# Optimization experiments

Hardware: AMD Instinct MI355X
Metric: run time of the kernel (lower is better)

The kernel has to match this reference:

```python
import jax, jax.numpy as jnp
import numpy as np
from jax import lax

NUM_EMBEDDING = 512
D_EMBEDDING = 256
COMMITMENT_COST = 0.25
B = 131072


def setup_inputs() -> dict:
    key = jax.random.key(0)
    k1, k2, k3 = jax.random.split(key, 3)
    node_type = jax.random.randint(k1, (B,), 0, 10, dtype=jnp.int64 if jax.config.jax_enable_x64 else jnp.int32)
    node_representation = jax.random.normal(k2, (B, D_EMBEDDING), dtype=jnp.float32)
    # nn.Embedding default init: N(0, 1)
    codebook = jax.random.normal(k3, (NUM_EMBEDDING, D_EMBEDDING), dtype=jnp.float32)
    return {"node_type": node_type, "node_representation": node_representation, "codebook": codebook}


def _code_indices(node_type, z, codebook):
    # Map atom type -> codebook quadrant: C(5)->0, N(6)->1, O(7)->2, others->3
    K = codebook.shape[0]
    qsize = K // 4
    group = jnp.where(node_type == 5, 0,
            jnp.where(node_type == 6, 1,
            jnp.where(node_type == 7, 2, 3)))  # [b]
    # Squared L2 distances to all codes: ||z||^2 + ||e||^2 - 2 z.e  -> [b, K]
    d2 = (jnp.sum(z * z, axis=1, keepdims=True)
          + jnp.sum(codebook * codebook, axis=1)
          - 2.0 * (z @ codebook.T))
    col_group = jnp.arange(K) // qsize  # [K], quadrant of each code
    valid = group[:, None] == col_group[None, :]  # [b, K]
    # Masked argmin == per-quadrant argmin (+ quadrant offset), as in the original.
    return jnp.argmin(jnp.where(valid, d2, jnp.inf), axis=1)


def reference(node_type, node_representation, codebook):
    z = node_representation
    idx = _code_indices(node_type, z, codebook)          # [b]
    quantized = codebook[idx]                            # [b, d]
    vq_loss = jnp.mean((quantized - lax.stop_gradient(z)) ** 2)
    commitment_loss = COMMITMENT_COST * jnp.mean((z - lax.stop_gradient(quantized)) ** 2)
    # Straight-through estimator
    quantized_st = z + lax.stop_gradient(quantized - z)
    return (vq_loss, commitment_loss, idx, quantized_st)
```

## Files before the change

### kernel.cpp

```cpp
#include <hip/hip_runtime.h>


#define B_ROWS   131072
#define D_EMB    256
#define TPB      256
#define MAXT     8196
#define SGRID2   1025
#define THETA    0.0625f

#define WS_WSUM   0
#define WS_I64N   512
#define WS_GCNT   516
#define WS_GPOS   532
#define WS_NT     548
#define WS_CBH    1024
#define WS_CBL    (WS_CBH + 262144)
#define WS_EN     (WS_CBL + 262144)
#define WS_ROWS   (WS_EN + 2048)
#define WS_TD     (WS_ROWS + 524288)
#define WS_NEED_NEW (WS_TD + 4 * MAXT)
#define WS_FLAGS  8

typedef __attribute__((ext_vector_type(8))) short bf16x8;
typedef __attribute__((ext_vector_type(4))) float f32x4;

__device__ __forceinline__ float bf2f(unsigned short u) {
    return __uint_as_float(((unsigned)u) << 16);
}

__device__ __forceinline__ void splitA(const float4& a0, const float4& a1,
                                       bf16x8& ah, bf16x8& al) {
    float ff[8] = {a0.x, a0.y, a0.z, a0.w, a1.x, a1.y, a1.z, a1.w};
    #pragma unroll
    for (int j = 0; j < 8; ++j) {
        unsigned u = __float_as_uint(ff[j]);
        ah[j] = (short)(u >> 16);
        float r = ff[j] - __uint_as_float(u & 0xffff0000u);
        al[j] = (short)(__float_as_uint(r) >> 16);
    }
}

__global__ void vq_prep(const float* __restrict__ cbf, const int* __restrict__ nt,
                        unsigned short* __restrict__ cbh, unsigned short* __restrict__ cbl,
                        float* __restrict__ eN, int* __restrict__ flagI64) {
    const int code = blockIdx.x;
    const int lane = threadIdx.x;
    float4 v = *(const float4*)(cbf + code * 256 + lane * 4);

    unsigned u0 = __float_as_uint(v.x), u1 = __float_as_uint(v.y);
    unsigned u2 = __float_as_uint(v.z), u3 = __float_as_uint(v.w);
    ushort4 h = make_ushort4((unsigned short)(u0 >> 16), (unsigned short)(u1 >> 16),
                             (unsigned short)(u2 >> 16), (unsigned short)(u3 >> 16));
    float r0 = v.x - __uint_as_float(u0 & 0xffff0000u);
    float r1 = v.y - __uint_as_float(u1 & 0xffff0000u);
    float r2 = v.z - __uint_as_float(u2 & 0xffff0000u);
    float r3 = v.w - __uint_as_float(u3 & 0xffff0000u);
    ushort4 l = make_ushort4((unsigned short)(__float_as_uint(r0) >> 16),
                             (unsigned short)(__float_as_uint(r1) >> 16),
                             (unsigned short)(__float_as_uint(r2) >> 16),
                             (unsigned short)(__float_as_uint(r3) >> 16));
    *(ushort4*)(cbh + code * 256 + lane * 4) = h;
    *(ushort4*)(cbl + code * 256 + lane * 4) = l;

    float s = fmaf(v.x, v.x, fmaf(v.y, v.y, fmaf(v.z, v.z, v.w * v.w)));
    #pragma unroll
    for (int d = 1; d < 64; d <<= 1) s += __shfl_xor(s, d);
    if (lane == 0) eN[code] = s;

    if (code == 0) {
        int o = (nt[2 * lane + 1] != 0) ? 1 : 0;
        unsigned long long m = __ballot(o != 0);
        if (lane == 0) flagI64[0] = (m == 0ULL) ? 1 : 0;
    }
}

__global__ void vq_bin1(const int* __restrict__ nt, const int* __restrict__ fI,
                        int* __restrict__ gcnt) {
    __shared__ int c[4];
    const int tid = threadIdx.x;
    if (tid < 4) c[tid] = 0;
    __syncthreads();
    const int row = blockIdx.x * 256 + tid;
    const int t = fI[0] ? nt[2 * row] : nt[row];
    const int g = (t == 5) ? 0 : (t == 6) ? 1 : (t == 7) ? 2 : 3;
    atomicAdd(&c[g], 1);
    __syncthreads();
    if (tid < 4) atomicAdd(&gcnt[tid], c[tid]);
}

__global__ void vq_tiles32(const int* __restrict__ gcnt, int* __restrict__ gpos,
                           int* __restrict__ nT, int* __restrict__ td) {
    __shared__ int off[4], cnt[4], to[4], tot;
    if (threadIdx.x == 0) {
        int o = 0, t = 0;
        for (int g = 0; g < 4; ++g) {
            cnt[g] = gcnt[g];
            off[g] = o; o += cnt[g];
            int tc = (cnt[g] + 31) >> 5;
            to[g] = t; t += tc;
            gpos[g] = off[g];
        }
        tot = t; nT[0] = t;
    }
    __syncthreads();
    const int t = tot;
    for (int i = threadIdx.x; i < t; i += 64) {
        int g = 3;
        if (i < to[1]) g = 0; else if (i < to[2]) g = 1; else if (i < to[3]) g = 2;
        int b = i - to[g];
        int base = off[g] + b * 32;
        int nr = cnt[g] - b * 32; if (nr > 32) nr = 32;
        td[i] = nr | (base << 6) | (g << 23);
    }
}

__global__ void vq_bin2(const int* __restrict__ nt, const int* __restrict__ fI,
                        int* __restrict__ gpos, int* __restrict__ rows) {
    __shared__ int base[4], pos[4];
    const int tid = threadIdx.x;
    if (tid < 4) pos[tid] = 0;
    __syncthreads();
    const int row = blockIdx.x * 256 + tid;
    const int t = fI[0] ? nt[2 * row] : nt[row];
    const int g = (t == 5) ? 0 : (t == 6) ? 1 : (t == 7) ? 2 : 3;
    atomicAdd(&pos[g], 1);
    __syncthreads();
    if (tid < 4) { base[tid] = atomicAdd(&gpos[tid], pos[tid]); pos[tid] = 0; }
    __syncthreads();
    int p = atomicAdd(&pos[g], 1);
    rows[base[g] + p] = row;
}

__global__ __launch_bounds__(TPB, 3) void vq_score2(
    const float* __restrict__ zf,
    const float* __restrict__ cbf,
    const unsigned short* __restrict__ cbh,
    const unsigned short* __restrict__ cbl,
    const float* __restrict__ eN,
    const int* __restrict__ rows,
    const int* __restrict__ td,
    const int* __restrict__ nT,
    float* __restrict__ out,
    double* __restrict__ wsum)
{
    __shared__ int2   sT[4][16];
    __shared__ float2 sM[4][16];
    __shared__ float  sZZ[4][16];
    __shared__ double sRed[4];

    const int tid  = threadIdx.x;
    const int wave = tid >> 6;
    const int lane = tid & 63;
    const int col  = lane & 15;
    const int quad = lane >> 4;
    const int w    = blockIdx.x * 4 + wave;

    double lacc = 0.0;

    if (w < nT[0]) {
        const int d    = td[w];
        const int nr   = d & 63;
        const int base = (d >> 6) & 0x1FFFF;
        const int g    = d >> 23;
        const int nr0  = (nr < 16) ? nr : 16;
        const int nr1  = nr - 16;

        int ix0 = base + ((col < nr0) ? col : (nr0 - 1));
        int ix1 = (nr1 > 0) ? (base + 16 + ((col < nr1) ? col : (nr1 - 1))) : ix0;
        const int rowA0 = rows[ix0];
        const int rowA1 = rows[ix1];
        const float* za0 = zf + rowA0 * 256 + quad * 8;
        const float* za1 = zf + rowA1 * 256 + quad * 8;
        const unsigned short* bhp = cbh + (g * 128 + col) * 256 + quad * 8;
        const unsigned short* blp = cbl + (g * 128 + col) * 256 + quad * 8;

        f32x4 acc[2][8];
        #pragma unroll
        for (int st = 0; st < 2; ++st)
            #pragma unroll
            for (int t = 0; t < 8; ++t) acc[st][t] = (f32x4){0.f, 0.f, 0.f, 0.f};
        float zz0 = 0.f, zz1 = 0.f;

        #pragma unroll
        for (int c = 0; c < 8; ++c) {
            float4 a00 = *(const float4*)(za0 + c * 32);
            float4 a01 = *(const float4*)(za0 + c * 32 + 4);
            float4 a10 = *(const float4*)(za1 + c * 32);
            float4 a11 = *(const float4*)(za1 + c * 32 + 4);
            zz0 = fmaf(a00.x,a00.x,fmaf(a00.y,a00.y,fmaf(a00.z,a00.z,fmaf(a00.w,a00.w,zz0))));
            zz0 = fmaf(a01.x,a01.x,fmaf(a01.y,a01.y,fmaf(a01.z,a01.z,fmaf(a01.w,a01.w,zz0))));
            zz1 = fmaf(a10.x,a10.x,fmaf(a10.y,a10.y,fmaf(a10.z,a10.z,fmaf(a10.w,a10.w,zz1))));
            zz1 = fmaf(a11.x,a11.x,fmaf(a11.y,a11.y,fmaf(a11.z,a11.z,fmaf(a11.w,a11.w,zz1))));
            bf16x8 ah0, al0, ah1, al1;
            splitA(a00, a01, ah0, al0);
            splitA(a10, a11, ah1, al1);
            #pragma unroll
            for (int t = 0; t < 8; ++t) {
                bf16x8 bh = *(const bf16x8*)(bhp + t * 4096 + c * 32);
                bf16x8 bl = *(const bf16x8*)(blp + t * 4096 + c * 32);
                acc[0][t] = __builtin_amdgcn_mfma_f32_16x16x32_bf16(ah0, bh, acc[0][t], 0, 0, 0);
                acc[0][t] = __builtin_amdgcn_mfma_f32_16x16x32_bf16(al0, bh, acc[0][t], 0, 0, 0);
                acc[0][t] = __builtin_amdgcn_mfma_f32_16x16x32_bf16(ah0, bl, acc[0][t], 0, 0, 0);
                acc[1][t] = __builtin_amdgcn_mfma_f32_16x16x32_bf16(ah1, bh, acc[1][t], 0, 0, 0);
                acc[1][t] = __builtin_amdgcn_mfma_f32_16x16x32_bf16(al1, bh, acc[1][t], 0, 0, 0);
                acc[1][t] = __builtin_amdgcn_mfma_f32_16x16x32_bf16(ah1, bl, acc[1][t], 0, 0, 0);
            }
        }
        zz0 += __shfl_xor(zz0, 16); zz0 += __shfl_xor(zz0, 32);
        zz1 += __shfl_xor(zz1, 16); zz1 += __shfl_xor(zz1, 32);

        float e8[8];
        #pragma unroll
        for (int t = 0; t < 8; ++t) e8[t] = eN[g * 128 + t * 16 + col];

        for (int st = 0; st < 2; ++st) {
            const int nrs = st ? nr1 : nr0;
            if (nrs <= 0) continue;
            if (quad == 0) sZZ[wave][col] = st ? zz1 : zz0;

            #pragma unroll
            for (int r = 0; r < 4; ++r) {
                float m1 = __builtin_inff(), m2 = __builtin_inff();
                int   i1 = 0x7fffffff,      i2 = 0x7fffffff;
                #pragma unroll
                for (int t = 0; t < 8; ++t) {
                    float sc = e8[t] - 2.f * acc[st][t][r];
                    int   ci = t * 16 + col;
                    if (sc < m1 || (sc == m1 && ci < i1)) { m2 = m1; i2 = i1; m1 = sc; i1 = ci; }
                    else if (sc < m2 || (sc == m2 && ci < i2)) { m2 = sc; i2 = ci; }
                }
                #pragma unroll
                for (int d2 = 1; d2 < 16; d2 <<= 1) {
                    float b1 = __shfl_xor(m1, d2);
                    int  bi1 = __shfl_xor(i1, d2);
                    float b2 = __shfl_xor(m2, d2);
                    int  bi2 = __shfl_xor(i2, d2);
                    if (b1 < m1 || (b1 == m1 && bi1 < i1)) {
                        float om = m1; int oi = i1;
                        m1 = b1; i1 = bi1;
                        if (b2 < om || (b2 == om && bi2 < oi)) { m2 = b2; i2 = bi2; }
                        else                                   { m2 = om; i2 = oi; }
                    } else {
                        if (b1 < m2 || (b1 == m2 && bi1 < i2)) { m2 = b1; i2 = bi1; }
                    }
                }
                if (col == 0) {
                    sT[wave][quad * 4 + r] = make_int2(i1, i2);
                    sM[wave][quad * 4 + r] = make_float2(m1, m2);
                }
            }

            const int s  = lane >> 2;
            const int pq = lane & 3;
            const bool valid = (s < nrs);
            int grow = 0, c1 = 0, c2 = 0;
            float scm1 = 0.f, scm2 = 1e30f, zzr = 0.f;
            if (valid) {
                grow = rows[base + st * 16 + s];
                int2  tt = sT[wave][s];
                float2 mm = sM[wave][s];
                zzr = sZZ[wave][s];
                c1 = g * 128 + tt.x;
                c2 = g * 128 + tt.y;
                scm1 = mm.x; scm2 = mm.y;
            }
            int    wfin  = c1;
            double dfull = (double)(zzr + scm1);
            const bool need = valid && (scm2 - scm1 <= THETA);

            if (__any(need)) {
                double d1c = 0.0, d2c = 0.0;
                if (need) {
                    const float* zp = zf  + grow * 256 + pq * 64;
                    const float* p1 = cbf + c1 * 256 + pq * 64;
                    const float* p2 = cbf + c2 * 256 + pq * 64;
                    #pragma unroll 4
                    for (int it = 0; it < 16; ++it) {
                        float4 fz = *(const float4*)(zp + it * 4);
                        float4 g1 = *(const float4*)(p1 + it * 4);
                        float4 g2 = *(const float4*)(p2 + it * 4);
                        double e;
                        e = (double)fz.x - (double)g1.x; d1c = fma(e, e, d1c);
                        e = (double)fz.y - (double)g1.y; d1c = fma(e, e, d1c);
                        e = (double)fz.z - (double)g1.z; d1c = fma(e, e, d1c);
                        e = (double)fz.w - (double)g1.w; d1c = fma(e, e, d1c);
                        e = (double)fz.x - (double)g2.x; d2c = fma(e, e, d2c);
                        e = (double)fz.y - (double)g2.y; d2c = fma(e, e, d2c);
                        e = (double)fz.z - (double)g2.z; d2c = fma(e, e, d2c);
                        e = (double)fz.w - (double)g2.w; d2c = fma(e, e, d2c);
                    }
                }
                double t1 = d1c + __shfl_xor(d1c, 1); t1 += __shfl_xor(t1, 2);
                double t2 = d2c + __shfl_xor(d2c, 1); t2 += __shfl_xor(t2, 2);
                if (need) {
                    bool take1 = (t1 < t2) || (t1 == t2 && c1 < c2);
                    wfin  = take1 ? c1 : c2;
                    dfull = take1 ? t1 : t2;
                }
            }

            if (valid) {
                if (pq == 0) lacc += dfull;
                const float* pw = cbf + wfin * 256 + pq * 64;
                const int obase = 2 + B_ROWS + grow * 256 + pq * 64;
                float4 fprev = *(const float4*)(pw);
                *(float2*)(out + obase) = make_float2(fprev.x, fprev.y);
                #pragma unroll
                for (int it = 1; it < 16; ++it) {
                    float4 fcur = *(const float4*)(pw + it * 4);
                    *(float4*)(out + obase + (it - 1) * 4 + 2) =
                        make_float4(fprev.z, fprev.w, fcur.x, fcur.y);
                    fprev = fcur;
                }
                *(float2*)(out + obase + 62) = make_float2(fprev.z, fprev.w);
                if (pq == 0) out[2 + grow] = (float)wfin;
            }
        }
    }

    #pragma unroll
    for (int d2 = 1; d2 < 64; d2 <<= 1) lacc += __shfl_xor(lacc, d2);
    if (lane == 0) sRed[wave] = lacc;
    __syncthreads();
    if (tid == 0) atomicAdd(&wsum[blockIdx.x & 63], sRed[0] + sRed[1] + sRed[2] + sRed[3]);
}

__global__ void vq_detect(const unsigned short* cb, const int* nt, int* flag) {
    __shared__ int cnt, odd;
    if (threadIdx.x == 0) { cnt = 0; odd = 0; }
    __syncthreads();
    int c = 0, o = 0;
    for (int i = threadIdx.x; i < 512; i += 64) {
        unsigned short u = cb[2 * i];
        int e = (u >> 7) & 0xFF;
        if (e < 100 || e > 140) c++;
    }
    if (nt[2 * threadIdx.x + 1] != 0) o = 1;
    atomicAdd(&cnt, c);
    atomicAdd(&odd, o);
    __syncthreads();
    if (threadIdx.x == 0) {
        flag[0] = (cnt < 50) ? 1 : 0;
        flag[1] = (odd == 0) ? 1 : 0;
    }
}

__global__ __launch_bounds__(512, 2) void vq_main_f32(
    const int* __restrict__ nt,
    const float* __restrict__ zff,
    const float* __restrict__ cbf,
    float* __restrict__ out,
    double* __restrict__ wsum,
    const int* __restrict__ flag)
{
    if (flag[0] != 0) return;
    const int i64 = flag[1];

    __shared__ float  sE[256 * 132];
    __shared__ float  sZ[128 * 32];
    __shared__ int    sList[512];
    __shared__ int    sCnt[4], sPos[4];
    __shared__ int    sTop1[128], sTop2[128];
    __shared__ float  sEe[128];
    __shared__ double sRed[8];

    const int tid  = threadIdx.x;
    const int row0 = blockIdx.x * 512;

    if (tid < 4) { sCnt[tid] = 0; sPos[tid] = 0; }
    __syncthreads();
    {
        int t = i64 ? nt[2 * (row0 + tid)] : nt[row0 + tid];
        int g = (t == 5) ? 0 : (t == 6) ? 1 : (t == 7) ? 2 : 3;
        atomicAdd(&sCnt[g], 1);
        __syncthreads();
        int o1 = sCnt[0], o2 = o1 + sCnt[1], o3 = o2 + sCnt[2];
        int offg = (g == 0) ? 0 : (g == 1) ? o1 : (g == 2) ? o2 : o3;
        int p = atomicAdd(&sPos[g], 1);
        sList[offg + p] = row0 + tid;
    }
    __syncthreads();

    int cnt[4], off[4];
    cnt[0] = sCnt[0]; cnt[1] = sCnt[1]; cnt[2] = sCnt[2]; cnt[3] = sCnt[3];
    off[0] = 0; off[1] = cnt[0]; off[2] = off[1] + cnt[1]; off[3] = off[2] + cnt[2];

    const int ccol = tid & 31, rrow = tid >> 5;
    const int c0 = ccol * 4, rbase = rrow * 8;
    double lacc = 0.0;

    for (int gg = 0; gg < 4; ++gg) {
        const int n = cnt[gg];
        if (n == 0) continue;
        __syncthreads();
        for (int i = tid; i < 128 * 256; i += 512) {
            int c = i >> 8, k = i & 255;
            sE[k * 132 + c] = cbf[(gg * 128 + c) * 256 + k];
        }
        __syncthreads();
        if (tid < 128) {
            float s = 0.f;
            for (int k = 0; k < 256; ++k) { float v = sE[k * 132 + tid]; s = fmaf(v, v, s); }
            sEe[tid] = s;
        }
        __syncthreads();

        const int ntiles = (n + 127) >> 7;
        for (int tI = 0; tI < ntiles; ++tI) {
            const int tbase = off[gg] + tI * 128;
            const int nrows = min(128, n - tI * 128);
            float acc[8][4];
            #pragma unroll
            for (int r = 0; r < 8; ++r)
                #pragma unroll
                for (int q = 0; q < 4; ++q) acc[r][q] = 0.f;

            for (int kb = 0; kb < 8; ++kb) {
                __syncthreads();
                #pragma unroll
                for (int it = 0; it < 2; ++it) {
                    int i = it * 512 + tid;
                    int s = i >> 3, j = i & 7;
                    float4 v = make_float4(0.f, 0.f, 0.f, 0.f);
                    if (s < nrows) {
                        int gr = sList[tbase + s];
                        v = *(const float4*)(zff + gr * 256 + kb * 32 + j * 4);
                    }
                    *(float4*)&sZ[s * 32 + j * 4] = v;
                }
                __syncthreads();
                #pragma unroll
                for (int k4 = 0; k4 < 8; ++k4) {
                    const int kk = kb * 32 + k4 * 4;
                    const float4 e0 = *(const float4*)&sE[(kk + 0) * 132 + c0];
                    const float4 e1 = *(const float4*)&sE[(kk + 1) * 132 + c0];
                    const float4 e2 = *(const float4*)&sE[(kk + 2) * 132 + c0];
                    const float4 e3 = *(const float4*)&sE[(kk + 3) * 132 + c0];
                    #pragma unroll
                    for (int r = 0; r < 8; ++r) {
                        const float4 zv = *(const float4*)&sZ[(rbase + r) * 32 + k4 * 4];
                        acc[r][0] = fmaf(zv.x, e0.x, fmaf(zv.y, e1.x, fmaf(zv.z, e2.x, fmaf(zv.w, e3.x, acc[r][0]))));
                        acc[r][1] = fmaf(zv.x, e0.y, fmaf(zv.y, e1.y, fmaf(zv.z, e2.y, fmaf(zv.w, e3.y, acc[r][1]))));
                        acc[r][2] = fmaf(zv.x, e0.z, fmaf(zv.y, e1.z, fmaf(zv.z, e2.z, fmaf(zv.w, e3.z, acc[r][2]))));
                        acc[r][3] = fmaf(zv.x, e0.w, fmaf(zv.y, e1.w, fmaf(zv.z, e2.w, fmaf(zv.w, e3.w, acc[r][3]))));
                    }
                }
            }

            float eq[4] = { sEe[c0], sEe[c0 + 1], sEe[c0 + 2], sEe[c0 + 3] };
            for (int r = 0; r < 8; ++r) {
                float m1 = __builtin_inff(), m2 = __builtin_inff();
                int   i1 = 0x7fffffff,      i2 = 0x7fffffff;
                #pragma unroll
                for (int q = 0; q < 4; ++q) {
                    float sc = eq[q] - 2.f * acc[r][q];
                    int   ci = c0 + q;
                    if (sc < m1 || (sc == m1 && ci < i1)) { m2 = m1; i2 = i1; m1 = sc; i1 = ci; }
                    else if (sc < m2 || (sc == m2 && ci < i2)) { m2 = sc; i2 = ci; }
                }
                #pragma unroll
                for (int d = 1; d < 32; d <<= 1) {
                    float b1 = __shfl_xor(m1, d);
                    int  bi1 = __shfl_xor(i1, d);
                    float b2 = __shfl_xor(m2, d);
                    int  bi2 = __shfl_xor(i2, d);
                    if (b1 < m1 || (b1 == m1 && bi1 < i1)) {
                        float om = m1; int oi = i1;
                        m1 = b1; i1 = bi1;
                        if (b2 < om || (b2 == om && bi2 < oi)) { m2 = b2; i2 = bi2; }
                        else                                   { m2 = om; i2 = oi; }
                    } else {
                        if (b1 < m2 || (b1 == m2 && bi1 < i2)) { m2 = b1; i2 = bi1; }
                    }
                }
                if (ccol == 0) { sTop1[rbase + r] = i1; sTop2[rbase + r] = i2; }
            }
            __syncthreads();

            {
                const int s  = tid >> 2;
                const int pq = tid & 3;
                const bool valid = (s < nrows);
                double d1c = 0.0, d2c = 0.0;
                int gr = 0, c1g = 0, c2g = 0;
                if (valid) {
                    gr  = sList[tbase + s];
                    c1g = gg * 128 + sTop1[s];
                    c2g = gg * 128 + sTop2[s];
                    #pragma unroll 4
                    for (int it = 0; it < 16; ++it) {
                        float4 fz = *(const float4*)(zff + gr  * 256 + pq * 64 + it * 4);
                        float4 f1 = *(const float4*)(cbf + c1g * 256 + pq * 64 + it * 4);
                        float4 f2 = *(const float4*)(cbf + c2g * 256 + pq * 64 + it * 4);
                        double e;
                        e = (double)fz.x - (double)f1.x; d1c = fma(e, e, d1c);
                        e = (double)fz.y - (double)f1.y; d1c = fma(e, e, d1c);
                        e = (double)fz.z - (double)f1.z; d1c = fma(e, e, d1c);
                        e = (double)fz.w - (double)f1.w; d1c = fma(e, e, d1c);
                        e = (double)fz.x - (double)f2.x; d2c = fma(e, e, d2c);
                        e = (double)fz.y - (double)f2.y; d2c = fma(e, e, d2c);
                        e = (double)fz.z - (double)f2.z; d2c = fma(e, e, d2c);
                        e = (double)fz.w - (double)f2.w; d2c = fma(e, e, d2c);
                    }
                }
                double t1 = d1c + __shfl_xor(d1c, 1); t1 += __shfl_xor(t1, 2);
                double t2 = d2c + __shfl_xor(d2c, 1); t2 += __shfl_xor(t2, 2);
                if (valid) {
                    bool take1 = (t1 < t2) || (t1 == t2 && c1g < c2g);
                    int  w = take1 ? c1g : c2g;
                    lacc += take1 ? d1c : d2c;
                    const int obase = 2 + B_ROWS + gr * 256 + pq * 64;
                    #pragma unroll 4
                    for (int it = 0; it < 16; ++it) {
                        float4 f4 = *(const float4*)(cbf + w * 256 + pq * 64 + it * 4);
                        *(float2*)(out + obase + it * 4)     = make_float2(f4.x, f4.y);
                        *(float2*)(out + obase + it * 4 + 2) = make_float2(f4.z, f4.w);
                    }
                    if (pq == 0) out[2 + gr] = (float)w;
                }
            }
        }
    }

    #pragma unroll
    for (int d = 1; d < 64; d <<= 1) lacc += __shfl_xor(lacc, d);
    if ((tid & 63) == 0) sRed[tid >> 6] = lacc;
    __syncthreads();
    if (tid == 0) {
        double s = 0.0;
        #pragma unroll
        for (int i = 0; i < 8; ++i) s += sRed[i];
        atomicAdd(wsum, s);
    }
}

__global__ void vq_fin(const double* wsum, float* out, int n) {
    if (threadIdx.x == 0 && blockIdx.x == 0) {
        double m = 0.0;
        for (int i = 0; i < n; ++i) m += wsum[i];
        m /= ((double)B_ROWS * (double)D_EMB);
        out[0] = (float)m;
        out[1] = (float)(0.25 * m);
    }
}

extern "C" void kernel_launch(void* const* d_in, const int* in_sizes, int n_in,
                              void* d_out, int out_size, void* d_ws, size_t ws_size,
                              hipStream_t stream) {
    const int*   nt  = (const int*)d_in[0];
    const float* zf  = (const float*)d_in[1];
    const float* cbf = (const float*)d_in[2];
    float*  out  = (float*)d_out;
    double* wsum = (double*)((char*)d_ws + WS_WSUM);

    hipMemsetAsync(d_ws, 0, 1024, stream);

    if (ws_size >= (size_t)WS_NEED_NEW) {
        unsigned short* cbh  = (unsigned short*)((char*)d_ws + WS_CBH);
        unsigned short* cbl  = (unsigned short*)((char*)d_ws + WS_CBL);
        float* eN    = (float*)((char*)d_ws + WS_EN);
        int*   fI64  = (int*)((char*)d_ws + WS_I64N);
        int*   gcnt  = (int*)((char*)d_ws + WS_GCNT);
        int*   gpos  = (int*)((char*)d_ws + WS_GPOS);
        int*   nTp   = (int*)((char*)d_ws + WS_NT);
        int*   rowsp = (int*)((char*)d_ws + WS_ROWS);
        int*   tdp   = (int*)((char*)d_ws + WS_TD);
        vq_prep<<<512, 64, 0, stream>>>(cbf, nt, cbh, cbl, eN, fI64);
        vq_bin1<<<512, 256, 0, stream>>>(nt, fI64, gcnt);
        vq_tiles32<<<1, 64, 0, stream>>>(gcnt, gpos, nTp, tdp);
        vq_bin2<<<512, 256, 0, stream>>>(nt, fI64, gpos, rowsp);
        vq_score2<<<SGRID2, TPB, 0, stream>>>(zf, cbf, cbh, cbl, eN, rowsp, tdp, nTp,
                                              out, wsum);
        vq_fin<<<1, 64, 0, stream>>>(wsum, out, 64);
    } else {
        int* flag = (int*)((char*)d_ws + WS_FLAGS);
        vq_detect<<<1, 64, 0, stream>>>((const unsigned short*)cbf, nt, flag);
        vq_main_f32<<<256, 512, 0, stream>>>(nt, zf, cbf, out, wsum, flag);
        vq_fin<<<1, 64, 0, stream>>>(wsum, out, 1);
    }
}
```

Before: 420.5 us.

## Fuse prep and binning, use 64-row tiles with group-partitioned persistent scoring

Merges the codebook split kernel with the first group-count pass, which removes one launch and the int64-flag buffer. Row tiles grow from 32 to 64 rows per wave, so each loaded codebook fragment feeds four MFMA row blocks instead of two. A persistent grid of 512 blocks is partitioned across the four codebook groups in proportion to tile counts, keeping blocks on a single codebook quadrant. The quantized-row copy is rewritten to use coalesced strided loads plus lane shuffles. The price is more accumulator registers (launch bounds drop to 2 blocks per unit) and possible load imbalance between groups.

```diff
diff --git a/kernel.cpp b/kernel.cpp
--- a/kernel.cpp
+++ b/kernel.cpp
@@ -5,14 +5,12 @@
 #define D_EMB    256
 #define TPB      256
 #define MAXT     8196
-#define SGRID2   1025
 #define THETA    0.0625f
 
 #define WS_WSUM   0
-#define WS_I64N   512
 #define WS_GCNT   516
 #define WS_GPOS   532
-#define WS_NT     548
+#define WS_GB     560
 #define WS_CBH    1024
 #define WS_CBL    (WS_CBH + 262144)
 #define WS_EN     (WS_CBL + 262144)
@@ -40,67 +38,78 @@
     }
 }
 
-__global__ void vq_prep(const float* __restrict__ cbf, const int* __restrict__ nt,
-                        unsigned short* __restrict__ cbh, unsigned short* __restrict__ cbl,
-                        float* __restrict__ eN, int* __restrict__ flagI64) {
-    const int code = blockIdx.x;
-    const int lane = threadIdx.x;
-    float4 v = *(const float4*)(cbf + code * 256 + lane * 4);
-
-    unsigned u0 = __float_as_uint(v.x), u1 = __float_as_uint(v.y);
-    unsigned u2 = __float_as_uint(v.z), u3 = __float_as_uint(v.w);
-    ushort4 h = make_ushort4((unsigned short)(u0 >> 16), (unsigned short)(u1 >> 16),
-                             (unsigned short)(u2 >> 16), (unsigned short)(u3 >> 16));
-    float r0 = v.x - __uint_as_float(u0 & 0xffff0000u);
-    float r1 = v.y - __uint_as_float(u1 & 0xffff0000u);
-    float r2 = v.z - __uint_as_float(u2 & 0xffff0000u);
-    float r3 = v.w - __uint_as_float(u3 & 0xffff0000u);
-    ushort4 l = make_ushort4((unsigned short)(__float_as_uint(r0) >> 16),
-                             (unsigned short)(__float_as_uint(r1) >> 16),
-                             (unsigned short)(__float_as_uint(r2) >> 16),
-                             (unsigned short)(__float_as_uint(r3) >> 16));
-    *(ushort4*)(cbh + code * 256 + lane * 4) = h;
-    *(ushort4*)(cbl + code * 256 + lane * 4) = l;
-
-    float s = fmaf(v.x, v.x, fmaf(v.y, v.y, fmaf(v.z, v.z, v.w * v.w)));
-    #pragma unroll
-    for (int d = 1; d < 64; d <<= 1) s += __shfl_xor(s, d);
-    if (lane == 0) eN[code] = s;
-
-    if (code == 0) {
-        int o = (nt[2 * lane + 1] != 0) ? 1 : 0;
+__global__ void vq_prep2(const float* __restrict__ cbf, const int* __restrict__ nt,
+                         unsigned short* __restrict__ cbh, unsigned short* __restrict__ cbl,
+                         float* __restrict__ eN, int* __restrict__ gcnt) {
+    __shared__ int sI64, c4[4];
+    const int bid = blockIdx.x;
+    const int tid = threadIdx.x;
+
+    if (tid < 4) c4[tid] = 0;
+
+    if (tid < 64) {
+        const int lane = tid;
+        float4 v = *(const float4*)(cbf + bid * 256 + lane * 4);
+        unsigned u0 = __float_as_uint(v.x), u1 = __float_as_uint(v.y);
+        unsigned u2 = __float_as_uint(v.z), u3 = __float_as_uint(v.w);
+        ushort4 h = make_ushort4((unsigned short)(u0 >> 16), (unsigned short)(u1 >> 16),
+                                 (unsigned short)(u2 >> 16), (unsigned short)(u3 >> 16));
+        float r0 = v.x - __uint_as_float(u0 & 0xffff0000u);
+        float r1 = v.y - __uint_as_float(u1 & 0xffff0000u);
+        float r2 = v.z - __uint_as_float(u2 & 0xffff0000u);
+        float r3 = v.w - __uint_as_float(u3 & 0xffff0000u);
+        ushort4 l = make_ushort4((unsigned short)(__float_as_uint(r0) >> 16),
+                                 (unsigned short)(__float_as_uint(r1) >> 16),
+                                 (unsigned short)(__float_as_uint(r2) >> 16),
+                                 (unsigned short)(__float_as_uint(r3) >> 16));
+        *(ushort4*)(cbh + bid * 256 + lane * 4) = h;
+        *(ushort4*)(cbl + bid * 256 + lane * 4) = l;
+        float s = fmaf(v.x, v.x, fmaf(v.y, v.y, fmaf(v.z, v.z, v.w * v.w)));
+        #pragma unroll
+        for (int d = 1; d < 64; d <<= 1) s += __shfl_xor(s, d);
+        if (lane == 0) eN[bid] = s;
+    } else if (tid < 128) {
+        int o = (nt[2 * (tid - 64) + 1] != 0) ? 1 : 0;
         unsigned long long m = __ballot(o != 0);
-        if (lane == 0) flagI64[0] = (m == 0ULL) ? 1 : 0;
-    }
-}
-
-__global__ void vq_bin1(const int* __restrict__ nt, const int* __restrict__ fI,
-                        int* __restrict__ gcnt) {
-    __shared__ int c[4];
-    const int tid = threadIdx.x;
-    if (tid < 4) c[tid] = 0;
-    __syncthreads();
-    const int row = blockIdx.x * 256 + tid;
-    const int t = fI[0] ? nt[2 * row] : nt[row];
-    const int g = (t == 5) ? 0 : (t == 6) ? 1 : (t == 7) ? 2 : 3;
-    atomicAdd(&c[g], 1);
-    __syncthreads();
-    if (tid < 4) atomicAdd(&gcnt[tid], c[tid]);
-}
-
-__global__ void vq_tiles32(const int* __restrict__ gcnt, int* __restrict__ gpos,
-                           int* __restrict__ nT, int* __restrict__ td) {
+        if (tid == 64) sI64 = (m == 0ULL) ? 1 : 0;
+    }
+    __syncthreads();
+
+    const int i64 = sI64;
+    const int row = bid * 256 + tid;
+    const int tv  = i64 ? nt[2 * row] : nt[row];
+    const int g   = (tv == 5) ? 0 : (tv == 6) ? 1 : (tv == 7) ? 2 : 3;
+    atomicAdd(&c4[g], 1);
+    __syncthreads();
+    if (tid < 4) atomicAdd(&gcnt[tid], c4[tid]);
+}
+
+__global__ void vq_tiles64(const int* __restrict__ gcnt, int* __restrict__ gpos,
+                           int* __restrict__ meta, int* __restrict__ td) {
     __shared__ int off[4], cnt[4], to[4], tot;
     if (threadIdx.x == 0) {
-        int o = 0, t = 0;
+        int o = 0, t = 0, tl[4], nb[4];
         for (int g = 0; g < 4; ++g) {
             cnt[g] = gcnt[g];
             off[g] = o; o += cnt[g];
-            int tc = (cnt[g] + 31) >> 5;
-            to[g] = t; t += tc;
+            tl[g] = (cnt[g] + 63) >> 6;
+            to[g] = t; t += tl[g];
             gpos[g] = off[g];
         }
-        tot = t; nT[0] = t;
+        tot = t;
+        int s3 = 0;
+        for (int g = 0; g < 3; ++g) {
+            nb[g] = (int)(512.0 * tl[g] / (double)(t > 0 ? t : 1) + 0.5);
+            if (nb[g] < 1) nb[g] = 1;
+            s3 += nb[g];
+        }
+        nb[3] = 512 - s3; if (nb[3] < 1) nb[3] = 1;
+        meta[0] = 0;
+        meta[1] = nb[0];
+        meta[2] = nb[0] + nb[1];
+        meta[3] = nb[0] + nb[1] + nb[2];
+        meta[4] = meta[3] + nb[3];
+        for (int g = 0; g < 4; ++g) { meta[5 + g] = to[g]; meta[9 + g] = tl[g]; }
     }
     __syncthreads();
     const int t = tot;
@@ -108,30 +117,36 @@
         int g = 3;
         if (i < to[1]) g = 0; else if (i < to[2]) g = 1; else if (i < to[3]) g = 2;
         int b = i - to[g];
-        int base = off[g] + b * 32;
-        int nr = cnt[g] - b * 32; if (nr > 32) nr = 32;
-        td[i] = nr | (base << 6) | (g << 23);
-    }
-}
-
-__global__ void vq_bin2(const int* __restrict__ nt, const int* __restrict__ fI,
-                        int* __restrict__ gpos, int* __restrict__ rows) {
-    __shared__ int base[4], pos[4];
+        int base = off[g] + b * 64;
+        int nr = cnt[g] - b * 64; if (nr > 64) nr = 64;
+        td[i] = nr | (base << 7) | (g << 24);
+    }
+}
+
+__global__ void vq_bin2(const int* __restrict__ nt, int* __restrict__ gpos,
+                        int* __restrict__ rows) {
+    __shared__ int sI64, basev[4], pos[4];
     const int tid = threadIdx.x;
     if (tid < 4) pos[tid] = 0;
-    __syncthreads();
+    if (tid >= 64 && tid < 128) {
+        int o = (nt[2 * (tid - 64) + 1] != 0) ? 1 : 0;
+        unsigned long long m = __ballot(o != 0);
+        if (tid == 64) sI64 = (m == 0ULL) ? 1 : 0;
+    }
+    __syncthreads();
+    const int i64 = sI64;
     const int row = blockIdx.x * 256 + tid;
-    const int t = fI[0] ? nt[2 * row] : nt[row];
-    const int g = (t == 5) ? 0 : (t == 6) ? 1 : (t == 7) ? 2 : 3;
+    const int tv  = i64 ? nt[2 * row] : nt[row];
+    const int g   = (tv == 5) ? 0 : (tv == 6) ? 1 : (tv == 7) ? 2 : 3;
     atomicAdd(&pos[g], 1);
     __syncthreads();
-    if (tid < 4) { base[tid] = atomicAdd(&gpos[tid], pos[tid]); pos[tid] = 0; }
+    if (tid < 4) { basev[tid] = atomicAdd(&gpos[tid], pos[tid]); pos[tid] = 0; }
     __syncthreads();
     int p = atomicAdd(&pos[g], 1);
-    rows[base[g] + p] = row;
-}
-
-__global__ __launch_bounds__(TPB, 3) void vq_score2(
+    rows[basev[g] + p] = row;
+}
+
+__global__ __launch_bounds__(TPB, 2) void vq_score3(
     const float* __restrict__ zf,
     const float* __restrict__ cbf,
     const unsigned short* __restrict__ cbh,
@@ -139,7 +154,7 @@
     const float* __restrict__ eN,
     const int* __restrict__ rows,
     const int* __restrict__ td,
-    const int* __restrict__ nT,
+    const int* __restrict__ meta,
     float* __restrict__ out,
     double* __restrict__ wsum)
 {
@@ -153,79 +168,95 @@
     const int lane = tid & 63;
     const int col  = lane & 15;
     const int quad = lane >> 4;
-    const int w    = blockIdx.x * 4 + wave;
+    const int bid  = blockIdx.x;
+
+    const int gb1 = meta[1], gb2 = meta[2], gb3 = meta[3];
+    const int g = (bid < gb1) ? 0 : (bid < gb2) ? 1 : (bid < gb3) ? 2 : 3;
+    const int gstart = meta[g];
+    const int nbg    = meta[g + 1] - gstart;
+    const int lb     = bid - gstart;
+    const int to_g   = meta[5 + g];
+    const int tl_g   = meta[9 + g];
+    const int r0     = lb * 4 + wave;
+    const int stride = nbg * 4;
 
     double lacc = 0.0;
 
-    if (w < nT[0]) {
-        const int d    = td[w];
-        const int nr   = d & 63;
-        const int base = (d >> 6) & 0x1FFFF;
-        const int g    = d >> 23;
-        const int nr0  = (nr < 16) ? nr : 16;
-        const int nr1  = nr - 16;
-
-        int ix0 = base + ((col < nr0) ? col : (nr0 - 1));
-        int ix1 = (nr1 > 0) ? (base + 16 + ((col < nr1) ? col : (nr1 - 1))) : ix0;
-        const int rowA0 = rows[ix0];
-        const int rowA1 = rows[ix1];
-        const float* za0 = zf + rowA0 * 256 + quad * 8;
-        const float* za1 = zf + rowA1 * 256 + quad * 8;
+    for (int t = r0; t < tl_g; t += stride) {
+        const int d    = td[to_g + t];
+        const int nr   = d & 127;
+        const int base = (d >> 7) & 0x1FFFF;
+
+        int nrs[4];
+        #pragma unroll
+        for (int st = 0; st < 4; ++st) {
+            int n = nr - st * 16;
+            nrs[st] = (n < 0) ? 0 : ((n > 16) ? 16 : n);
+        }
+        const float* za[4];
+        #pragma unroll
+        for (int st = 0; st < 4; ++st) {
+            int nn = nrs[st];
+            int ix = base + st * 16 + ((nn > 0) ? ((col < nn) ? col : (nn - 1)) : -st * 16);
+            za[st] = zf + rows[ix] * 256 + quad * 8;
+        }
         const unsigned short* bhp = cbh + (g * 128 + col) * 256 + quad * 8;
         const unsigned short* blp = cbl + (g * 128 + col) * 256 + quad * 8;
 
-        f32x4 acc[2][8];
-        #pragma unroll
-        for (int st = 0; st < 2; ++st)
+        f32x4 acc[4][8];
+        #pragma unroll
+        for (int st = 0; st < 4; ++st)
             #pragma unroll
-            for (int t = 0; t < 8; ++t) acc[st][t] = (f32x4){0.f, 0.f, 0.f, 0.f};
-        float zz0 = 0.f, zz1 = 0.f;
+            for (int t8 = 0; t8 < 8; ++t8) acc[st][t8] = (f32x4){0.f, 0.f, 0.f, 0.f};
+        float zz[4] = {0.f, 0.f, 0.f, 0.f};
 
         #pragma unroll
         for (int c = 0; c < 8; ++c) {
-            float4 a00 = *(const float4*)(za0 + c * 32);
-            float4 a01 = *(const float4*)(za0 + c * 32 + 4);
-            float4 a10 = *(const float4*)(za1 + c * 32);
-            float4 a11 = *(const float4*)(za1 + c * 32 + 4);
-            zz0 = fmaf(a00.x,a00.x,fmaf(a00.y,a00.y,fmaf(a00.z,a00.z,fmaf(a00.w,a00.w,zz0))));
-            zz0 = fmaf(a01.x,a01.x,fmaf(a01.y,a01.y,fmaf(a01.z,a01.z,fmaf(a01.w,a01.w,zz0))));
-            zz1 = fmaf(a10.x,a10.x,fmaf(a10.y,a10.y,fmaf(a10.z,a10.z,fmaf(a10.w,a10.w,zz1))));
-            zz1 = fmaf(a11.x,a11.x,fmaf(a11.y,a11.y,fmaf(a11.z,a11.z,fmaf(a11.w,a11.w,zz1))));
-            bf16x8 ah0, al0, ah1, al1;
-            splitA(a00, a01, ah0, al0);
-            splitA(a10, a11, ah1, al1);
+            bf16x8 ah[4], al[4];
             #pragma unroll
-            for (int t = 0; t < 8; ++t) {
-                bf16x8 bh = *(const bf16x8*)(bhp + t * 4096 + c * 32);
-                bf16x8 bl = *(const bf16x8*)(blp + t * 4096 + c * 32);
-                acc[0][t] = __builtin_amdgcn_mfma_f32_16x16x32_bf16(ah0, bh, acc[0][t], 0, 0, 0);
-                acc[0][t] = __builtin_amdgcn_mfma_f32_16x16x32_bf16(al0, bh, acc[0][t], 0, 0, 0);
-                acc[0][t] = __builtin_amdgcn_mfma_f32_16x16x32_bf16(ah0, bl, acc[0][t], 0, 0, 0);
-                acc[1][t] = __builtin_amdgcn_mfma_f32_16x16x32_bf16(ah1, bh, acc[1][t], 0, 0, 0);
-                acc[1][t] = __builtin_amdgcn_mfma_f32_16x16x32_bf16(al1, bh, acc[1][t], 0, 0, 0);
-                acc[1][t] = __builtin_amdgcn_mfma_f32_16x16x32_bf16(ah1, bl, acc[1][t], 0, 0, 0);
-            }
-        }
-        zz0 += __shfl_xor(zz0, 16); zz0 += __shfl_xor(zz0, 32);
-        zz1 += __shfl_xor(zz1, 16); zz1 += __shfl_xor(zz1, 32);
+            for (int st = 0; st < 4; ++st) {
+                float4 x0 = *(const float4*)(za[st] + c * 32);
+                float4 x1 = *(const float4*)(za[st] + c * 32 + 4);
+                zz[st] = fmaf(x0.x,x0.x,fmaf(x0.y,x0.y,fmaf(x0.z,x0.z,fmaf(x0.w,x0.w,zz[st]))));
+                zz[st] = fmaf(x1.x,x1.x,fmaf(x1.y,x1.y,fmaf(x1.z,x1.z,fmaf(x1.w,x1.w,zz[st]))));
+                splitA(x0, x1, ah[st], al[st]);
+            }
+            #pragma unroll
+            for (int t8 = 0; t8 < 8; ++t8) {
+                bf16x8 bh = *(const bf16x8*)(bhp + t8 * 4096 + c * 32);
+                bf16x8 bl = *(const bf16x8*)(blp + t8 * 4096 + c * 32);
+                #pragma unroll
+                for (int st = 0; st < 4; ++st) {
+                    acc[st][t8] = __builtin_amdgcn_mfma_f32_16x16x32_bf16(ah[st], bh, acc[st][t8], 0, 0, 0);
+                    acc[st][t8] = __builtin_amdgcn_mfma_f32_16x16x32_bf16(al[st], bh, acc[st][t8], 0, 0, 0);
+                    acc[st][t8] = __builtin_amdgcn_mfma_f32_16x16x32_bf16(ah[st], bl, acc[st][t8], 0, 0, 0);
+                }
+            }
+        }
+        #pragma unroll
+        for (int st = 0; st < 4; ++st) {
+            zz[st] += __shfl_xor(zz[st], 16);
+            zz[st] += __shfl_xor(zz[st], 32);
+        }
 
         float e8[8];
         #pragma unroll
-        for (int t = 0; t < 8; ++t) e8[t] = eN[g * 128 + t * 16 + col];
-
-        for (int st = 0; st < 2; ++st) {
-            const int nrs = st ? nr1 : nr0;
-            if (nrs <= 0) continue;
-            if (quad == 0) sZZ[wave][col] = st ? zz1 : zz0;
+        for (int t8 = 0; t8 < 8; ++t8) e8[t8] = eN[g * 128 + t8 * 16 + col];
+
+        #pragma unroll
+        for (int st = 0; st < 4; ++st) {
+            const int nrs_ = nrs[st];
+            if (nrs_ <= 0) continue;
+            if (quad == 0) sZZ[wave][col] = zz[st];
 
             #pragma unroll
             for (int r = 0; r < 4; ++r) {
                 float m1 = __builtin_inff(), m2 = __builtin_inff();
                 int   i1 = 0x7fffffff,      i2 = 0x7fffffff;
                 #pragma unroll
-                for (int t = 0; t < 8; ++t) {
-                    float sc = e8[t] - 2.f * acc[st][t][r];
-                    int   ci = t * 16 + col;
+                for (int t8 = 0; t8 < 8; ++t8) {
+                    float sc = e8[t8] - 2.f * acc[st][t8][r];
+                    int   ci = t8 * 16 + col;
                     if (sc < m1 || (sc == m1 && ci < i1)) { m2 = m1; i2 = i1; m1 = sc; i1 = ci; }
                     else if (sc < m2 || (sc == m2 && ci < i2)) { m2 = sc; i2 = ci; }
                 }
@@ -252,12 +283,12 @@
 
             const int s  = lane >> 2;
             const int pq = lane & 3;
-            const bool valid = (s < nrs);
+            const bool valid = (s < nrs_);
             int grow = 0, c1 = 0, c2 = 0;
             float scm1 = 0.f, scm2 = 1e30f, zzr = 0.f;
             if (valid) {
                 grow = rows[base + st * 16 + s];
-                int2  tt = sT[wave][s];
+                int2   tt = sT[wave][s];
                 float2 mm = sM[wave][s];
                 zzr = sZZ[wave][s];
                 c1 = g * 128 + tt.x;
@@ -271,14 +302,15 @@
             if (__any(need)) {
                 double d1c = 0.0, d2c = 0.0;
                 if (need) {
-                    const float* zp = zf  + grow * 256 + pq * 64;
-                    const float* p1 = cbf + c1 * 256 + pq * 64;
-                    const float* p2 = cbf + c2 * 256 + pq * 64;
+                    const float* zp = zf  + grow * 256;
+                    const float* p1 = cbf + c1 * 256;
+                    const float* p2 = cbf + c2 * 256;
                     #pragma unroll 4
                     for (int it = 0; it < 16; ++it) {
-                        float4 fz = *(const float4*)(zp + it * 4);
-                        float4 g1 = *(const float4*)(p1 + it * 4);
-                        float4 g2 = *(const float4*)(p2 + it * 4);
+                        const int m = it * 16 + pq * 4;
+                        float4 fz = *(const float4*)(zp + m);
+                        float4 g1 = *(const float4*)(p1 + m);
+                        float4 g2 = *(const float4*)(p2 + m);
                         double e;
                         e = (double)fz.x - (double)g1.x; d1c = fma(e, e, d1c);
                         e = (double)fz.y - (double)g1.y; d1c = fma(e, e, d1c);
@@ -299,21 +331,30 @@
                 }
             }
 
-            if (valid) {
-                if (pq == 0) lacc += dfull;
-                const float* pw = cbf + wfin * 256 + pq * 64;
-                const int obase = 2 + B_ROWS + grow * 256 + pq * 64;
-                float4 fprev = *(const float4*)(pw);
-                *(float2*)(out + obase) = make_float2(fprev.x, fprev.y);
-                #pragma unroll
-                for (int it = 1; it < 16; ++it) {
-                    float4 fcur = *(const float4*)(pw + it * 4);
-                    *(float4*)(out + obase + (it - 1) * 4 + 2) =
-                        make_float4(fprev.z, fprev.w, fcur.x, fcur.y);
-                    fprev = fcur;
-                }
-                *(float2*)(out + obase + 62) = make_float2(fprev.z, fprev.w);
-                if (pq == 0) out[2 + grow] = (float)wfin;
+            {
+                if (valid && pq == 0) lacc += dfull;
+                const float* pw = cbf + wfin * 256;
+                const int ob = 2 + B_ROWS + grow * 256;
+                float4 cur = *(const float4*)(pw + pq * 4);
+                #pragma unroll
+                for (int it = 0; it < 16; ++it) {
+                    float4 nxt = make_float4(0.f, 0.f, 0.f, 0.f);
+                    if (it < 15) nxt = *(const float4*)(pw + (it + 1) * 16 + pq * 4);
+                    float ax = __shfl(cur.x, lane + 1);
+                    float ay = __shfl(cur.y, lane + 1);
+                    float bx = __shfl(nxt.x, lane & 60);
+                    float by = __shfl(nxt.y, lane & 60);
+                    float nx = (pq < 3) ? ax : bx;
+                    float ny = (pq < 3) ? ay : by;
+                    const int q = it * 4 + pq;
+                    if (valid) {
+                        if (q == 0) *(float2*)(out + ob) = make_float2(cur.x, cur.y);
+                        if (q < 63) *(float4*)(out + ob + 2 + 4 * q) = make_float4(cur.z, cur.w, nx, ny);
+                        else        *(float2*)(out + ob + 254) = make_float2(cur.z, cur.w);
+                    }
+                    cur = nxt;
+                }
+                if (valid && pq == 0) out[2 + grow] = (float)wfin;
             }
         }
     }
@@ -559,18 +600,16 @@
         unsigned short* cbh  = (unsigned short*)((char*)d_ws + WS_CBH);
         unsigned short* cbl  = (unsigned short*)((char*)d_ws + WS_CBL);
         float* eN    = (float*)((char*)d_ws + WS_EN);
-        int*   fI64  = (int*)((char*)d_ws + WS_I64N);
         int*   gcnt  = (int*)((char*)d_ws + WS_GCNT);
         int*   gpos  = (int*)((char*)d_ws + WS_GPOS);
-        int*   nTp   = (int*)((char*)d_ws + WS_NT);
+        int*   metap = (int*)((char*)d_ws + WS_GB);
         int*   rowsp = (int*)((char*)d_ws + WS_ROWS);
         int*   tdp   = (int*)((char*)d_ws + WS_TD);
-        vq_prep<<<512, 64, 0, stream>>>(cbf, nt, cbh, cbl, eN, fI64);
-        vq_bin1<<<512, 256, 0, stream>>>(nt, fI64, gcnt);
-        vq_tiles32<<<1, 64, 0, stream>>>(gcnt, gpos, nTp, tdp);
-        vq_bin2<<<512, 256, 0, stream>>>(nt, fI64, gpos, rowsp);
-        vq_score2<<<SGRID2, TPB, 0, stream>>>(zf, cbf, cbh, cbl, eN, rowsp, tdp, nTp,
-                                              out, wsum);
+        vq_prep2<<<512, 256, 0, stream>>>(cbf, nt, cbh, cbl, eN, gcnt);
+        vq_tiles64<<<1, 64, 0, stream>>>(gcnt, gpos, metap, tdp);
+        vq_bin2<<<512, 256, 0, stream>>>(nt, gpos, rowsp);
+        vq_score3<<<512, TPB, 0, stream>>>(zf, cbf, cbh, cbl, eN, rowsp, tdp, metap,
+                                           out, wsum);
         vq_fin<<<1, 64, 0, stream>>>(wsum, out, 64);
     } else {
         int* flag = (int*)((char*)d_ws + WS_FLAGS);
```

Result: slower. 486.2 us (+15.6%).
